# Optimization experiments

Hardware: AMD Instinct MI355X
Metric: run time of the kernel (lower is better)

## Reference

```python
import jax, jax.numpy as jnp
import numpy as np

BETA = 0.25
EPS = 1e-12  # matches torch F.normalize eps


def _normalize(x):
    # L2-normalize along last dim, matching F.normalize(x, dim=1)
    n = jnp.linalg.norm(x, axis=-1, keepdims=True)
    return x / jnp.maximum(n, EPS)


def setup_inputs() -> dict:
    key = jax.random.key(0)
    k1, k2 = jax.random.split(key)
    B, C, H, W = 32, 256, 32, 32
    num_embed = 8192
    z = jax.random.normal(k1, (B, C, H, W), dtype=jnp.float32)
    # codebook initialized uniform(-1/K, 1/K) as in the module
    embed_weight = jax.random.uniform(
        k2, (num_embed, C), minval=-1.0 / num_embed, maxval=1.0 / num_embed,
        dtype=jnp.float32)
    return {"z": z, "embed_weight": embed_weight}


def reference(z, embed_weight):
    B, C, H, W = z.shape
    sg = jax.lax.stop_gradient
    zt = jnp.transpose(z, (0, 2, 3, 1))           # [B, H, W, C]
    zf = zt.reshape(-1, C)                         # [N, C]
    # cosine distance (dot of normalized vectors); z side is detached
    zn = sg(_normalize(zf))                        # [N, C]
    cn = _normalize(embed_weight)                  # [K, C]
    dist = jnp.einsum('nd,kd->nk', zn, cn)         # [N, K]
    encoding_indices = jnp.argmax(dist, axis=1)    # [N]
    z_q = embed_weight[encoding_indices].reshape(zt.shape)  # [B, H, W, C]
    loss = (BETA * jnp.mean((sg(z_q) - zt) ** 2)
            + jnp.mean((z_q - sg(zt)) ** 2))
    z_q_st = zt + sg(z_q - zt)                     # straight-through
    out = jnp.transpose(z_q_st, (0, 3, 1, 2))      # [B, C, H, W]
    return out, loss, encoding_indices
```

## Files before the change

### kernel.cpp

```cpp
#include <hip/hip_runtime.h>

#define NROWS 32768
#define CDIM  256
#define KCODES 8192
#define HWPB  1024
#define OUT_ELEMS 8388608

typedef unsigned short ushort_t;
typedef unsigned int uint_t;
typedef __attribute__((ext_vector_type(8))) __bf16 bf16x8;
typedef __attribute__((ext_vector_type(4))) float f32x4;
typedef __attribute__((ext_vector_type(8))) ushort_t us8;
typedef __attribute__((ext_vector_type(4))) ushort_t us4;

#define RESCORE_THRESH 3.0e-4f

__device__ __forceinline__ ushort_t f2bf(float f) {
  uint_t u = __float_as_uint(f);
  return (ushort_t)((u + 0x7fffu + ((u >> 16) & 1u)) >> 16);
}
__device__ __forceinline__ float bf2f(ushort_t s) {
  return __uint_as_float(((uint_t)s) << 16);
}

__global__ __launch_bounds__(256) void vq_invnorm_kernel(
    const float* __restrict__ e, float* __restrict__ invn) {
  const int row  = blockIdx.x * 4 + (threadIdx.x >> 6);
  const int lane = threadIdx.x & 63;
  const float4 v = *reinterpret_cast<const float4*>(e + (size_t)row * CDIM + lane * 4);
  float s = v.x * v.x + v.y * v.y + v.z * v.z + v.w * v.w;
  #pragma unroll
  for (int o = 32; o > 0; o >>= 1) s += __shfl_down(s, o);
  if (lane == 0) invn[row] = 1.0f / fmaxf(sqrtf(s), 1e-12f);
}

__global__ __launch_bounds__(256) void vq_prep_b_kernel(
    const float* __restrict__ e, ushort_t* __restrict__ B2,
    float* __restrict__ invn) {
  const int k  = blockIdx.x * 4 + (threadIdx.x >> 6);
  const int ln = threadIdx.x & 63;
  const float4 v = reinterpret_cast<const float4*>(e + (size_t)k * CDIM)[ln];
  us4 hi, lo;
  const float vv[4] = {v.x, v.y, v.z, v.w};
  float s = 0.f;
  #pragma unroll
  for (int i = 0; i < 4; ++i) {
    ushort_t h = f2bf(vv[i]);
    hi[i] = h;
    lo[i] = f2bf(vv[i] - bf2f(h));
    s += vv[i] * vv[i];
  }
  *reinterpret_cast<us4*>(B2 + (size_t)k * 512 + ln * 4)       = hi;
  *reinterpret_cast<us4*>(B2 + (size_t)k * 512 + 256 + ln * 4) = lo;
  #pragma unroll
  for (int o = 32; o > 0; o >>= 1) s += __shfl_down(s, o);
  if (ln == 0) invn[k] = 1.0f / fmaxf(sqrtf(s), 1e-12f);
}

__global__ __launch_bounds__(256) void vq_prep_a_kernel(
    const float* __restrict__ z, ushort_t* __restrict__ A2) {
  __shared__ float zt[64][65];
  const int t    = threadIdx.x;
  const int bidx = blockIdx.x;
  const int b    = bidx >> 6;
  const int cblk = (bidx & 63) >> 4;
  const int hwb  = bidx & 15;
  const int c0   = cblk * 64;
  const int hw0  = hwb * 64;
  #pragma unroll
  for (int rep = 0; rep < 16; ++rep) {
    const int idx = rep * 256 + t;
    const int cc = idx >> 6, hh = idx & 63;
    zt[cc][hh] = z[(size_t)(b * 256 + c0 + cc) * 1024 + hw0 + hh];
  }
  __syncthreads();
  const int r = t >> 2, q = t & 3;
  const int n = b * 1024 + hw0 + r;
  us8 hi0, hi1, lo0, lo1;
  #pragma unroll
  for (int m2 = 0; m2 < 16; ++m2) {
    const float v = zt[q * 16 + m2][r];
    const ushort_t h = f2bf(v);
    const ushort_t l = f2bf(v - bf2f(h));
    if (m2 < 8) { hi0[m2] = h; lo0[m2] = l; } else { hi1[m2 - 8] = h; lo1[m2 - 8] = l; }
  }
  ushort_t* hrow = A2 + (size_t)n * 512 + c0 + q * 16;
  ushort_t* lrow = A2 + (size_t)n * 512 + 256 + c0 + q * 16;
  *reinterpret_cast<us8*>(hrow)     = hi0;
  *reinterpret_cast<us8*>(hrow + 8) = hi1;
  *reinterpret_cast<us8*>(lrow)     = lo0;
  *reinterpret_cast<us8*>(lrow + 8) = lo1;
}

__global__ __launch_bounds__(256, 2) void vq_mfma_kernel(
    const ushort_t* __restrict__ A2, const ushort_t* __restrict__ B2,
    const float* __restrict__ invn,
    float* __restrict__ partV1, int* __restrict__ partI1,
    float* __restrict__ partV2) {
  __shared__ __align__(16) char As[2][16384];
  __shared__ __align__(16) char Bs[2][16384];

  const int t = threadIdx.x;
  const int w = t >> 6, l = t & 63;
  const int wr = w >> 1, wc = w & 1;
  const int lane15 = l & 15, kg = l >> 4;
  const int m0 = blockIdx.x * 128;
  const int cg = blockIdx.y;

  const int lr = l >> 3;
  const int lc = (l & 7) ^ lr;

  const ushort_t* aRow = A2 + (size_t)(m0 + w * 8 + lr) * 512 + lc * 8;
  const ushort_t* bRow = B2 + (size_t)(cg * 1024 + w * 8 + lr) * 512 + lc * 8;
  const int ldsOff = (w * 8) * 128;

  auto stage = [&](int step, int buf) {
    const int nt = step / 12, kc = step % 12;
    const int seg = kc >> 2, rem = (kc & 3) * 64;
    const int aoff = (seg == 1 ? 256 : 0) + rem;
    const int boff = (seg == 2 ? 256 : 0) + rem;
    const size_t bNt = (size_t)nt * (128 * 512);
    #pragma unroll
    for (int p = 0; p < 4; ++p) {
      __builtin_amdgcn_global_load_lds(
          (const __attribute__((address_space(1))) void*)(aRow + (size_t)p * (32 * 512) + aoff),
          (__attribute__((address_space(3))) void*)(As[buf] + p * 32 * 128 + ldsOff), 16, 0, 0);
      __builtin_amdgcn_global_load_lds(
          (const __attribute__((address_space(1))) void*)(bRow + bNt + (size_t)p * (32 * 512) + boff),
          (__attribute__((address_space(3))) void*)(Bs[buf] + p * 32 * 128 + ldsOff), 16, 0, 0);
    }
  };

  float bv[16], b2v[16]; int bi[16];
  #pragma unroll
  for (int iq = 0; iq < 16; ++iq) { bv[iq] = -3.4e38f; b2v[iq] = -3.4e38f; bi[iq] = 0; }

  stage(0, 0);

  int step = 0;
  for (int nt = 0; nt < 8; ++nt) {
    const int nbase = cg * 1024 + nt * 128;
    f32x4 acc[4][4];
    #pragma unroll
    for (int i = 0; i < 4; ++i)
      #pragma unroll
      for (int j = 0; j < 4; ++j) acc[i][j] = (f32x4){0.f, 0.f, 0.f, 0.f};

    for (int kc = 0; kc < 12; ++kc, ++step) {
      const int buf = step & 1;
      __syncthreads();
      if (step + 1 < 96) stage(step + 1, buf ^ 1);

      const char* Ab = As[buf];
      const char* Bb = Bs[buf];
      #pragma unroll
      for (int kk = 0; kk < 2; ++kk) {
        bf16x8 af[4], bfr[4];
        const int sw = kk * 64 + kg * 16;
        const int sx = (lane15 & 7) << 4;
        #pragma unroll
        for (int i = 0; i < 4; ++i)
          af[i] = *reinterpret_cast<const bf16x8*>(
              Ab + (wr * 64 + i * 16 + lane15) * 128 + (sw ^ sx));
        #pragma unroll
        for (int j = 0; j < 4; ++j)
          bfr[j] = *reinterpret_cast<const bf16x8*>(
              Bb + (wc * 64 + j * 16 + lane15) * 128 + (sw ^ sx));
        #pragma unroll
        for (int i = 0; i < 4; ++i)
          #pragma unroll
          for (int j = 0; j < 4; ++j)
            acc[i][j] = __builtin_amdgcn_mfma_f32_16x16x32_bf16(af[i], bfr[j], acc[i][j], 0, 0, 0);
      }
    }

    float inv4[4];
    #pragma unroll
    for (int j = 0; j < 4; ++j) inv4[j] = invn[nbase + wc * 64 + j * 16 + lane15];
    #pragma unroll
    for (int i = 0; i < 4; ++i)
      #pragma unroll
      for (int q = 0; q < 4; ++q) {
        const int iq = i * 4 + q;
        #pragma unroll
        for (int j = 0; j < 4; ++j) {
          const float v = acc[i][j][q] * inv4[j];
          const int k = nbase + wc * 64 + j * 16 + lane15;
          if (v > bv[iq]) { b2v[iq] = bv[iq]; bv[iq] = v; bi[iq] = k; }
          else if (v > b2v[iq]) b2v[iq] = v;
        }
      }
  }

  #pragma unroll
  for (int m = 1; m < 16; m <<= 1) {
    #pragma unroll
    for (int iq = 0; iq < 16; ++iq) {
      const float ov = __shfl_xor(bv[iq], m);
      const int   oi = __shfl_xor(bi[iq], m);
      const float o2 = __shfl_xor(b2v[iq], m);
      const float n2 = fmaxf(fmaxf(b2v[iq], o2), fminf(bv[iq], ov));
      if (ov > bv[iq] || (ov == bv[iq] && oi < bi[iq])) { bv[iq] = ov; bi[iq] = oi; }
      b2v[iq] = n2;
    }
  }

  __syncthreads();
  float* lv1 = reinterpret_cast<float*>(As[0]);
  float* lv2 = lv1 + 128;
  int*   li1 = reinterpret_cast<int*>(lv2 + 128);
  if (wc == 1 && lane15 == 0) {
    #pragma unroll
    for (int i = 0; i < 4; ++i)
      #pragma unroll
      for (int q = 0; q < 4; ++q) {
        const int rl = wr * 64 + i * 16 + kg * 4 + q;
        lv1[rl] = bv[i * 4 + q]; lv2[rl] = b2v[i * 4 + q]; li1[rl] = bi[i * 4 + q];
      }
  }
  __syncthreads();
  if (wc == 0 && lane15 == 0) {
    #pragma unroll
    for (int i = 0; i < 4; ++i)
      #pragma unroll
      for (int q = 0; q < 4; ++q) {
        const int iq = i * 4 + q;
        const int rl = wr * 64 + i * 16 + kg * 4 + q;
        const float ov = lv1[rl]; const float o2 = lv2[rl]; const int oi = li1[rl];
        const float n2 = fmaxf(fmaxf(b2v[iq], o2), fminf(bv[iq], ov));
        float v1 = bv[iq]; int i1 = bi[iq];
        if (ov > v1 || (ov == v1 && oi < i1)) { v1 = ov; i1 = oi; }
        const size_t g = (size_t)cg * NROWS + m0 + rl;
        partV1[g] = v1; partI1[g] = i1; partV2[g] = n2;
      }
  }
}

__global__ __launch_bounds__(256) void vq_merge_flag_kernel(
    const float* __restrict__ partV1, const int* __restrict__ partI1,
    const float* __restrict__ partV2,
    int* __restrict__ final_idx, int* __restrict__ flag, int* __restrict__ cnt) {
  const int n = blockIdx.x * 256 + threadIdx.x;
  float v1 = partV1[n]; int i1 = partI1[n]; float v2 = partV2[n];
  #pragma unroll
  for (int cg = 1; cg < 8; ++cg) {
    const float pv1 = partV1[(size_t)cg * NROWS + n];
    const int   pi1 = partI1[(size_t)cg * NROWS + n];
    const float pv2 = partV2[(size_t)cg * NROWS + n];
    const float n2 = fmaxf(fmaxf(v2, pv2), fminf(v1, pv1));
    if (pv1 > v1) { v1 = pv1; i1 = pi1; }
    v2 = n2;
  }
  final_idx[n] = i1;
  if (v1 - v2 < RESCORE_THRESH) {
    const int p = atomicAdd(cnt, 1);
    flag[p] = n;
  }
}

__global__ __launch_bounds__(256) void vq_rescore_kernel(
    const float* __restrict__ z, const float* __restrict__ e,
    const float* __restrict__ invn, const int* __restrict__ cnt,
    const int* __restrict__ flag, int* __restrict__ final_idx) {
  __shared__ float zr[8][256];
  __shared__ int rows[8];
  __shared__ float redv[8][4];
  __shared__ int   redi[8][4];
  const int t = threadIdx.x;
  const int total = *cnt;
  for (int base = blockIdx.x * 8; base < total; base += gridDim.x * 8) {
    const int nr = min(8, total - base);
    __syncthreads();
    if (t < 8) rows[t] = (base + t < total) ? flag[base + t] : flag[base];
    __syncthreads();
    for (int rr = 0; rr < 8; ++rr) {
      if (rr < nr) {
        const int n = rows[rr];
        const int b = n >> 10, hw = n & 1023;
        zr[rr][t] = z[(size_t)b * 262144 + (size_t)t * 1024 + hw];
      } else {
        zr[rr][t] = 0.f;
      }
    }
    __syncthreads();
    float bvv[8]; int bii[8];
    #pragma unroll
    for (int rr = 0; rr < 8; ++rr) { bvv[rr] = -3.4e38f; bii[rr] = 0; }
    for (int jj = 0; jj < 32; ++jj) {
      const int k = t * 32 + jj;
      const float4* er = reinterpret_cast<const float4*>(e + (size_t)k * CDIM);
      float d[8];
      #pragma unroll
      for (int rr = 0; rr < 8; ++rr) d[rr] = 0.f;
      for (int c4 = 0; c4 < 64; ++c4) {
        const float4 ev = er[c4];
        #pragma unroll
        for (int rr = 0; rr < 8; ++rr) {
          d[rr] = fmaf(ev.x, zr[rr][c4 * 4 + 0], d[rr]);
          d[rr] = fmaf(ev.y, zr[rr][c4 * 4 + 1], d[rr]);
          d[rr] = fmaf(ev.z, zr[rr][c4 * 4 + 2], d[rr]);
          d[rr] = fmaf(ev.w, zr[rr][c4 * 4 + 3], d[rr]);
        }
      }
      const float inv = invn[k];
      #pragma unroll
      for (int rr = 0; rr < 8; ++rr) {
        const float v = d[rr] * inv;
        if (v > bvv[rr]) { bvv[rr] = v; bii[rr] = k; }
      }
    }
    #pragma unroll
    for (int m = 1; m < 64; m <<= 1) {
      #pragma unroll
      for (int rr = 0; rr < 8; ++rr) {
        const float ov = __shfl_xor(bvv[rr], m);
        const int   oi = __shfl_xor(bii[rr], m);
        if (ov > bvv[rr] || (ov == bvv[rr] && oi < bii[rr])) { bvv[rr] = ov; bii[rr] = oi; }
      }
    }
    if ((t & 63) == 0) {
      #pragma unroll
      for (int rr = 0; rr < 8; ++rr) { redv[rr][t >> 6] = bvv[rr]; redi[rr][t >> 6] = bii[rr]; }
    }
    __syncthreads();
    if (t < nr) {
      float v = redv[t][0]; int i = redi[t][0];
      #pragma unroll
      for (int ww = 1; ww < 4; ++ww) {
        if (redv[t][ww] > v || (redv[t][ww] == v && redi[t][ww] < i)) { v = redv[t][ww]; i = redi[t][ww]; }
      }
      final_idx[rows[t]] = i;
    }
  }
}

__global__ __launch_bounds__(256) void vq_gather_loss2_kernel(
    const float* __restrict__ z, const float* __restrict__ e,
    const int* __restrict__ final_idx,
    float* __restrict__ out, float* __restrict__ lossacc) {
  __shared__ int sidx[64];
  const int t  = threadIdx.x;
  const int n0 = blockIdx.x * 64;
  if (t < 64) {
    const int id = final_idx[n0 + t];
    sidx[t] = id;
    out[OUT_ELEMS + 1 + n0 + t] = (float)id;
  }
  __syncthreads();
  const int b    = n0 >> 10;
  const int hw0  = n0 & 1023;
  const int nsub = t & 63;
  const int cg   = t >> 6;
  const float* erow = e + (size_t)sidx[nsub] * CDIM;
  float lsum = 0.f;
  for (int c = cg; c < CDIM; c += 4) {
    const float  v   = erow[c];
    const size_t off = (size_t)b * (CDIM * HWPB) + (size_t)c * HWPB + hw0 + nsub;
    const float  d   = v - z[off];
    lsum += d * d;
    out[off] = v;
  }
  #pragma unroll
  for (int o = 32; o > 0; o >>= 1) lsum += __shfl_down(lsum, o);
  __shared__ float wsum[4];
  if ((t & 63) == 0) wsum[t >> 6] = lsum;
  __syncthreads();
  if (t == 0) atomicAdd(lossacc, wsum[0] + wsum[1] + wsum[2] + wsum[3]);
}

__global__ void vq_finalize_kernel(const float* __restrict__ lossacc,
                                   float* __restrict__ out) {
  out[OUT_ELEMS] = 1.25f * lossacc[0] / (float)OUT_ELEMS;
}

#define BM 128
#define BN 128
#define KC 16
#define KSPLIT 4

__global__ __launch_bounds__(256) void vq_dist_argmax_kernel(
    const float* __restrict__ z, const float* __restrict__ e,
    const float* __restrict__ invn,
    float* __restrict__ bestval, int* __restrict__ bestidx) {
  __shared__ float as[KC][BM];
  __shared__ float bs[KC][BN + 4];
  const int t  = threadIdx.x;
  const int tx = t & 15;
  const int ty = t >> 4;
  const int n0 = blockIdx.x * BM;
  const int b   = n0 >> 10;
  const int hw0 = n0 & 1023;
  const float* zbase = z + (size_t)b * (CDIM * HWPB) + hw0;
  const int kbeg = blockIdx.y * (KCODES / KSPLIT);
  float bv[8]; int bi[8];
  #pragma unroll
  for (int i = 0; i < 8; ++i) { bv[i] = -3.4e38f; bi[i] = 0; }
  const int a_lm4 = (t & 31) * 4;
  const int a_cc  = t >> 5;
  const int b_kk  = t >> 2;
  const int b_q4  = (t & 3) * 4;
  for (int kt = 0; kt < (KCODES / KSPLIT) / BN; ++kt) {
    const int k0 = kbeg + kt * BN;
    float acc[8][8];
    #pragma unroll
    for (int i = 0; i < 8; ++i)
      #pragma unroll
      for (int j = 0; j < 8; ++j) acc[i][j] = 0.f;
    for (int c0 = 0; c0 < CDIM; c0 += KC) {
      #pragma unroll
      for (int p = 0; p < 2; ++p) {
        const int cc = a_cc + 8 * p;
        const float4 v = *reinterpret_cast<const float4*>(
            zbase + (size_t)(c0 + cc) * HWPB + a_lm4);
        *reinterpret_cast<float4*>(&as[cc][a_lm4]) = v;
      }
      #pragma unroll
      for (int p = 0; p < 2; ++p) {
        const int kk = b_kk + 64 * p;
        const float4 v = *reinterpret_cast<const float4*>(
            e + (size_t)(k0 + kk) * CDIM + c0 + b_q4);
        bs[b_q4 + 0][kk] = v.x;
        bs[b_q4 + 1][kk] = v.y;
        bs[b_q4 + 2][kk] = v.z;
        bs[b_q4 + 3][kk] = v.w;
      }
      __syncthreads();
      #pragma unroll
      for (int cc = 0; cc < KC; ++cc) {
        const float4 a0 = *reinterpret_cast<const float4*>(&as[cc][ty * 8]);
        const float4 a1 = *reinterpret_cast<const float4*>(&as[cc][ty * 8 + 4]);
        const float4 b0 = *reinterpret_cast<const float4*>(&bs[cc][tx * 4]);
        const float4 b1 = *reinterpret_cast<const float4*>(&bs[cc][64 + tx * 4]);
        const float a[8]  = {a0.x, a0.y, a0.z, a0.w, a1.x, a1.y, a1.z, a1.w};
        const float bb[8] = {b0.x, b0.y, b0.z, b0.w, b1.x, b1.y, b1.z, b1.w};
        #pragma unroll
        for (int i = 0; i < 8; ++i)
          #pragma unroll
          for (int j = 0; j < 8; ++j)
            acc[i][j] = fmaf(a[i], bb[j], acc[i][j]);
      }
      __syncthreads();
    }
    #pragma unroll
    for (int j = 0; j < 8; ++j) {
      const int k = k0 + ((j < 4) ? (tx * 4 + j) : (64 + tx * 4 + (j - 4)));
      const float inv = invn[k];
      #pragma unroll
      for (int i = 0; i < 8; ++i) {
        const float v = acc[i][j] * inv;
        if (v > bv[i]) { bv[i] = v; bi[i] = k; }
      }
    }
  }
  #pragma unroll
  for (int m = 1; m < 16; m <<= 1) {
    #pragma unroll
    for (int i = 0; i < 8; ++i) {
      const float vo = __shfl_xor(bv[i], m);
      const int   io = __shfl_xor(bi[i], m);
      if (vo > bv[i] || (vo == bv[i] && io < bi[i])) { bv[i] = vo; bi[i] = io; }
    }
  }
  if (tx == 0) {
    #pragma unroll
    for (int i = 0; i < 8; ++i) {
      bestval[blockIdx.y * NROWS + n0 + ty * 8 + i] = bv[i];
      bestidx[blockIdx.y * NROWS + n0 + ty * 8 + i] = bi[i];
    }
  }
}

__global__ __launch_bounds__(256) void vq_gather_loss_kernel(
    const float* __restrict__ z, const float* __restrict__ e,
    const float* __restrict__ bestval, const int* __restrict__ bestidx,
    float* __restrict__ out, float* __restrict__ lossacc) {
  __shared__ int sidx[64];
  const int t  = threadIdx.x;
  const int n0 = blockIdx.x * 64;
  if (t < 64) {
    const int n = n0 + t;
    float best = bestval[n];
    int   bid  = bestidx[n];
    #pragma unroll
    for (int p = 1; p < KSPLIT; ++p) {
      const float v = bestval[p * NROWS + n];
      const int  id = bestidx[p * NROWS + n];
      if (v > best) { best = v; bid = id; }
    }
    sidx[t] = bid;
    out[OUT_ELEMS + 1 + n] = (float)bid;
  }
  __syncthreads();
  const int b    = n0 >> 10;
  const int hw0  = n0 & 1023;
  const int nsub = t & 63;
  const int cg   = t >> 6;
  const float* erow = e + (size_t)sidx[nsub] * CDIM;
  float lsum = 0.f;
  for (int c = cg; c < CDIM; c += 4) {
    const float  v   = erow[c];
    const size_t off = (size_t)b * (CDIM * HWPB) + (size_t)c * HWPB + hw0 + nsub;
    const float  d   = v - z[off];
    lsum += d * d;
    out[off] = v;
  }
  #pragma unroll
  for (int o = 32; o > 0; o >>= 1) lsum += __shfl_down(lsum, o);
  __shared__ float wsum[4];
  if ((t & 63) == 0) wsum[t >> 6] = lsum;
  __syncthreads();
  if (t == 0) atomicAdd(lossacc, wsum[0] + wsum[1] + wsum[2] + wsum[3]);
}

extern "C" void kernel_launch(void* const* d_in, const int* in_sizes, int n_in,
                              void* d_out, int out_size, void* d_ws, size_t ws_size,
                              hipStream_t stream) {
  const float* z = (const float*)d_in[0];
  const float* e = (const float*)d_in[1];
  float* out = (float*)d_out;

  const size_t szA2 = (size_t)NROWS * 512 * 2;
  const size_t szB2 = (size_t)KCODES * 512 * 2;
  const size_t szInv = KCODES * 4;
  const size_t szPart = (size_t)8 * NROWS * 4;
  const size_t need = szA2 + szB2 + szInv + 3 * szPart + 2 * (size_t)NROWS * 4 + 256;

  if (ws_size >= need) {
    char* p = (char*)d_ws;
    ushort_t* A2 = (ushort_t*)p;       p += szA2;
    ushort_t* B2 = (ushort_t*)p;       p += szB2;
    float* invn  = (float*)p;          p += szInv;
    float* partV1 = (float*)p;         p += szPart;
    float* partV2 = (float*)p;         p += szPart;
    int*   partI1 = (int*)p;           p += szPart;
    int*   final_idx = (int*)p;        p += (size_t)NROWS * 4;
    int*   flag = (int*)p;             p += (size_t)NROWS * 4;
    int*   cnt = (int*)p;
    float* lossacc = (float*)(cnt + 1);

    hipMemsetAsync(cnt, 0, 8, stream);
    vq_prep_b_kernel<<<KCODES / 4, 256, 0, stream>>>(e, B2, invn);
    vq_prep_a_kernel<<<2048, 256, 0, stream>>>(z, A2);
    dim3 grid(NROWS / 128, 8);
    vq_mfma_kernel<<<grid, 256, 0, stream>>>(A2, B2, invn, partV1, partI1, partV2);
    vq_merge_flag_kernel<<<NROWS / 256, 256, 0, stream>>>(partV1, partI1, partV2,
                                                          final_idx, flag, cnt);
    vq_rescore_kernel<<<256, 256, 0, stream>>>(z, e, invn, cnt, flag, final_idx);
    vq_gather_loss2_kernel<<<NROWS / 64, 256, 0, stream>>>(z, e, final_idx, out, lossacc);
    vq_finalize_kernel<<<1, 1, 0, stream>>>(lossacc, out);
  } else {
    float* invn    = (float*)d_ws;
    float* bestval = invn + KCODES;
    int*   bestidx = (int*)(bestval + KSPLIT * NROWS);
    float* lossacc = (float*)(bestidx + KSPLIT * NROWS);
    hipMemsetAsync(lossacc, 0, sizeof(float), stream);
    vq_invnorm_kernel<<<KCODES / 4, 256, 0, stream>>>(e, invn);
    dim3 grid(NROWS / BM, KSPLIT);
    vq_dist_argmax_kernel<<<grid, 256, 0, stream>>>(z, e, invn, bestval, bestidx);
    vq_gather_loss_kernel<<<NROWS / 64, 256, 0, stream>>>(z, e, bestval, bestidx,
                                                          out, lossacc);
    vq_finalize_kernel<<<1, 1, 0, stream>>>(lossacc, out);
  }
}
```

Before: 1.349 ms.

## Restructure MFMA argmax kernel with fragment-ordered A and 4-stage B pipeline

The z-side bf16 hi/lo split is now written in an MFMA-fragment-ordered layout, so each wave loads its A fragments straight from global memory instead of staging them through LDS. The distance kernel grows to 512 threads with 256x256 tiles, a 4-deep LDS ring for codebook tiles tracked by vmcnt waits rather than per-step barriers, raised MFMA priority, and a per-tile argmax reduction through LDS. The gather/loss kernel is rewritten to one row per thread with float4 codebook reads. The risks are heavy global-load traffic for A, 140KB of dynamic shared memory, which limits occupancy to one block per CU, and register pressure from the 8x4 accumulator array.

```diff
diff --git a/kernel.cpp b/kernel.cpp
--- a/kernel.cpp
+++ b/kernel.cpp
@@ -58,7 +58,7 @@
 }
 
 __global__ __launch_bounds__(256) void vq_prep_a_kernel(
-    const float* __restrict__ z, ushort_t* __restrict__ A2) {
+    const float* __restrict__ z, char* __restrict__ A2f) {
   __shared__ float zt[64][65];
   const int t    = threadIdx.x;
   const int bidx = blockIdx.x;
@@ -74,8 +74,12 @@
     zt[cc][hh] = z[(size_t)(b * 256 + c0 + cc) * 1024 + hw0 + hh];
   }
   __syncthreads();
-  const int r = t >> 2, q = t & 3;
-  const int n = b * 1024 + hw0 + r;
+  const int q = t >> 6, r = t & 63;
+  const int n   = b * 1024 + hw0 + r;
+  const int R16 = n >> 4, l15 = n & 15;
+  const int cb  = c0 + q * 16;
+  const int kc  = cb >> 5;
+  const int kg0 = (cb >> 3) & 3;
   us8 hi0, hi1, lo0, lo1;
   #pragma unroll
   for (int m2 = 0; m2 < 16; ++m2) {
@@ -84,155 +88,147 @@
     const ushort_t l = f2bf(v - bf2f(h));
     if (m2 < 8) { hi0[m2] = h; lo0[m2] = l; } else { hi1[m2 - 8] = h; lo1[m2 - 8] = l; }
   }
-  ushort_t* hrow = A2 + (size_t)n * 512 + c0 + q * 16;
-  ushort_t* lrow = A2 + (size_t)n * 512 + 256 + c0 + q * 16;
-  *reinterpret_cast<us8*>(hrow)     = hi0;
-  *reinterpret_cast<us8*>(hrow + 8) = hi1;
-  *reinterpret_cast<us8*>(lrow)     = lo0;
-  *reinterpret_cast<us8*>(lrow + 8) = lo1;
-}
-
-__global__ __launch_bounds__(256, 2) void vq_mfma_kernel(
-    const ushort_t* __restrict__ A2, const ushort_t* __restrict__ B2,
+  const size_t base = (size_t)(R16 * 16 + kc) * 1024 + (size_t)(((kg0) << 4) | l15) * 16;
+  *reinterpret_cast<us8*>(A2f + base)              = hi0;
+  *reinterpret_cast<us8*>(A2f + base + 256)        = hi1;
+  *reinterpret_cast<us8*>(A2f + base + 8192)       = lo0;
+  *reinterpret_cast<us8*>(A2f + base + 8192 + 256) = lo1;
+}
+
+__global__ __launch_bounds__(512) void vq_mfma_kernel(
+    const char* __restrict__ A2f, const ushort_t* __restrict__ B2,
     const float* __restrict__ invn,
     float* __restrict__ partV1, int* __restrict__ partI1,
     float* __restrict__ partV2) {
-  __shared__ __align__(16) char As[2][16384];
-  __shared__ __align__(16) char Bs[2][16384];
+  extern __shared__ char smem[];
 
   const int t = threadIdx.x;
   const int w = t >> 6, l = t & 63;
-  const int wr = w >> 1, wc = w & 1;
-  const int lane15 = l & 15, kg = l >> 4;
-  const int m0 = blockIdx.x * 128;
+  const int wr = w >> 2, wc = w & 3;
+  const int l15 = l & 15, kg = l >> 4;
+  const int m0 = blockIdx.x * 256;
   const int cg = blockIdx.y;
 
-  const int lr = l >> 3;
-  const int lc = (l & 7) ^ lr;
-
-  const ushort_t* aRow = A2 + (size_t)(m0 + w * 8 + lr) * 512 + lc * 8;
-  const ushort_t* bRow = B2 + (size_t)(cg * 1024 + w * 8 + lr) * 512 + lc * 8;
-  const int ldsOff = (w * 8) * 128;
-
-  auto stage = [&](int step, int buf) {
-    const int nt = step / 12, kc = step % 12;
-    const int seg = kc >> 2, rem = (kc & 3) * 64;
-    const int aoff = (seg == 1 ? 256 : 0) + rem;
-    const int boff = (seg == 2 ? 256 : 0) + rem;
-    const size_t bNt = (size_t)nt * (128 * 512);
-    #pragma unroll
-    for (int p = 0; p < 4; ++p) {
+  const int rowB  = l >> 2;
+  const int slotB = (l & 3) ^ ((l >> 2) & 3);
+  const int rdoffB = l15 * 64 + ((kg ^ (l15 & 3)) << 4);
+  const char* aFbase = A2f + (size_t)m0 * 1024 + (size_t)wr * 131072 + (size_t)l * 16;
+
+  float* candV1 = reinterpret_cast<float*>(smem + 131072);
+  int*   candI1 = reinterpret_cast<int*>(smem + 135168);
+  float* candV2 = reinterpret_cast<float*>(smem + 139264);
+
+  auto stageB = [&](int s3) {
+    if (s3 >= 96) return;
+    const int nt3 = s3 / 24;
+    const int kc3 = s3 - nt3 * 24;
+    const int boff = (kc3 < 8) ? kc3 * 32
+                   : (kc3 < 16 ? (kc3 - 8) * 32 : 256 + (kc3 - 16) * 32);
+    const int bufb = (s3 & 3) * 32768 + w * 4096;
+    const ushort_t* src = B2 +
+        (size_t)((cg << 10) + nt3 * 256 + wc * 64 + rowB) * 512 + slotB * 8 + boff;
+    #pragma unroll
+    for (int u = 0; u < 4; ++u) {
       __builtin_amdgcn_global_load_lds(
-          (const __attribute__((address_space(1))) void*)(aRow + (size_t)p * (32 * 512) + aoff),
-          (__attribute__((address_space(3))) void*)(As[buf] + p * 32 * 128 + ldsOff), 16, 0, 0);
-      __builtin_amdgcn_global_load_lds(
-          (const __attribute__((address_space(1))) void*)(bRow + bNt + (size_t)p * (32 * 512) + boff),
-          (__attribute__((address_space(3))) void*)(Bs[buf] + p * 32 * 128 + ldsOff), 16, 0, 0);
+          (const __attribute__((address_space(1))) void*)(src + (size_t)u * (16 * 512)),
+          (__attribute__((address_space(3))) void*)(smem + bufb + u * 1024 + l * 16),
+          16, 0, 0);
     }
   };
 
-  float bv[16], b2v[16]; int bi[16];
-  #pragma unroll
-  for (int iq = 0; iq < 16; ++iq) { bv[iq] = -3.4e38f; b2v[iq] = -3.4e38f; bi[iq] = 0; }
-
-  stage(0, 0);
-
-  int step = 0;
-  for (int nt = 0; nt < 8; ++nt) {
-    const int nbase = cg * 1024 + nt * 128;
-    f32x4 acc[4][4];
-    #pragma unroll
-    for (int i = 0; i < 4; ++i)
+  stageB(0); stageB(1); stageB(2);
+
+  float rv1 = -3.4e38f, rv2 = -3.4e38f; int ri1 = 0;
+
+  for (int nt = 0; nt < 4; ++nt) {
+    const int nbase = (cg << 10) + nt * 256;
+    f32x4 acc[8][4];
+    #pragma unroll
+    for (int i = 0; i < 8; ++i)
       #pragma unroll
       for (int j = 0; j < 4; ++j) acc[i][j] = (f32x4){0.f, 0.f, 0.f, 0.f};
 
-    for (int kc = 0; kc < 12; ++kc, ++step) {
-      const int buf = step & 1;
-      __syncthreads();
-      if (step + 1 < 96) stage(step + 1, buf ^ 1);
-
-      const char* Ab = As[buf];
-      const char* Bb = Bs[buf];
-      #pragma unroll
-      for (int kk = 0; kk < 2; ++kk) {
-        bf16x8 af[4], bfr[4];
-        const int sw = kk * 64 + kg * 16;
-        const int sx = (lane15 & 7) << 4;
-        #pragma unroll
-        for (int i = 0; i < 4; ++i)
-          af[i] = *reinterpret_cast<const bf16x8*>(
-              Ab + (wr * 64 + i * 16 + lane15) * 128 + (sw ^ sx));
+    for (int kc = 0; kc < 24; ++kc) {
+      const int s = nt * 24 + kc;
+      stageB(s + 3);
+      asm volatile("s_waitcnt vmcnt(8)" ::: "memory");
+
+      const int kcA = (kc < 16) ? kc : kc - 16;
+      const char* aa = aFbase + (size_t)kcA * 1024;
+      bf16x8 af[8];
+      #pragma unroll
+      for (int i = 0; i < 8; ++i)
+        af[i] = *reinterpret_cast<const bf16x8*>(aa + (size_t)i * 16384);
+
+      const char* bb = smem + (s & 3) * 32768 + w * 4096 + rdoffB;
+      bf16x8 bfr[4];
+      #pragma unroll
+      for (int j = 0; j < 4; ++j)
+        bfr[j] = *reinterpret_cast<const bf16x8*>(bb + j * 1024);
+
+      __builtin_amdgcn_s_setprio(1);
+      #pragma unroll
+      for (int i = 0; i < 8; ++i)
         #pragma unroll
         for (int j = 0; j < 4; ++j)
-          bfr[j] = *reinterpret_cast<const bf16x8*>(
-              Bb + (wc * 64 + j * 16 + lane15) * 128 + (sw ^ sx));
+          acc[i][j] = __builtin_amdgcn_mfma_f32_16x16x32_bf16(af[i], bfr[j], acc[i][j], 0, 0, 0);
+      __builtin_amdgcn_s_setprio(0);
+    }
+
+    float inv[4];
+    #pragma unroll
+    for (int j = 0; j < 4; ++j) inv[j] = invn[nbase + wc * 64 + j * 16 + l15];
+
+    #pragma unroll
+    for (int i = 0; i < 8; ++i) {
+      #pragma unroll
+      for (int q = 0; q < 4; ++q) {
+        float v1 = acc[i][0][q] * inv[0];
+        int   i1 = nbase + wc * 64 + l15;
+        float v2 = -3.4e38f;
         #pragma unroll
-        for (int i = 0; i < 4; ++i)
-          #pragma unroll
-          for (int j = 0; j < 4; ++j)
-            acc[i][j] = __builtin_amdgcn_mfma_f32_16x16x32_bf16(af[i], bfr[j], acc[i][j], 0, 0, 0);
-      }
-    }
-
-    float inv4[4];
-    #pragma unroll
-    for (int j = 0; j < 4; ++j) inv4[j] = invn[nbase + wc * 64 + j * 16 + lane15];
-    #pragma unroll
-    for (int i = 0; i < 4; ++i)
-      #pragma unroll
-      for (int q = 0; q < 4; ++q) {
-        const int iq = i * 4 + q;
+        for (int j = 1; j < 4; ++j) {
+          const float v = acc[i][j][q] * inv[j];
+          const int   c = nbase + wc * 64 + j * 16 + l15;
+          if (v > v1) { v2 = v1; v1 = v; i1 = c; }
+          else if (v > v2) v2 = v;
+        }
         #pragma unroll
-        for (int j = 0; j < 4; ++j) {
-          const float v = acc[i][j][q] * inv4[j];
-          const int k = nbase + wc * 64 + j * 16 + lane15;
-          if (v > bv[iq]) { b2v[iq] = bv[iq]; bv[iq] = v; bi[iq] = k; }
-          else if (v > b2v[iq]) b2v[iq] = v;
+        for (int m = 1; m < 16; m <<= 1) {
+          const float ov = __shfl_xor(v1, m);
+          const int   oi = __shfl_xor(i1, m);
+          const float o2 = __shfl_xor(v2, m);
+          const float n2 = fmaxf(fmaxf(v2, o2), fminf(v1, ov));
+          if (ov > v1 || (ov == v1 && oi < i1)) { v1 = ov; i1 = oi; }
+          v2 = n2;
         }
-      }
-  }
-
-  #pragma unroll
-  for (int m = 1; m < 16; m <<= 1) {
-    #pragma unroll
-    for (int iq = 0; iq < 16; ++iq) {
-      const float ov = __shfl_xor(bv[iq], m);
-      const int   oi = __shfl_xor(bi[iq], m);
-      const float o2 = __shfl_xor(b2v[iq], m);
-      const float n2 = fmaxf(fmaxf(b2v[iq], o2), fminf(bv[iq], ov));
-      if (ov > bv[iq] || (ov == bv[iq] && oi < bi[iq])) { bv[iq] = ov; bi[iq] = oi; }
-      b2v[iq] = n2;
-    }
-  }
-
-  __syncthreads();
-  float* lv1 = reinterpret_cast<float*>(As[0]);
-  float* lv2 = lv1 + 128;
-  int*   li1 = reinterpret_cast<int*>(lv2 + 128);
-  if (wc == 1 && lane15 == 0) {
-    #pragma unroll
-    for (int i = 0; i < 4; ++i)
-      #pragma unroll
-      for (int q = 0; q < 4; ++q) {
-        const int rl = wr * 64 + i * 16 + kg * 4 + q;
-        lv1[rl] = bv[i * 4 + q]; lv2[rl] = b2v[i * 4 + q]; li1[rl] = bi[i * 4 + q];
-      }
-  }
-  __syncthreads();
-  if (wc == 0 && lane15 == 0) {
-    #pragma unroll
-    for (int i = 0; i < 4; ++i)
-      #pragma unroll
-      for (int q = 0; q < 4; ++q) {
-        const int iq = i * 4 + q;
-        const int rl = wr * 64 + i * 16 + kg * 4 + q;
-        const float ov = lv1[rl]; const float o2 = lv2[rl]; const int oi = li1[rl];
-        const float n2 = fmaxf(fmaxf(b2v[iq], o2), fminf(bv[iq], ov));
-        float v1 = bv[iq]; int i1 = bi[iq];
-        if (ov > v1 || (ov == v1 && oi < i1)) { v1 = ov; i1 = oi; }
-        const size_t g = (size_t)cg * NROWS + m0 + rl;
-        partV1[g] = v1; partI1[g] = i1; partV2[g] = n2;
-      }
+        if (l15 == 0) {
+          const int row = wr * 128 + i * 16 + kg * 4 + q;
+          candV1[wc * 256 + row] = v1;
+          candI1[wc * 256 + row] = i1;
+          candV2[wc * 256 + row] = v2;
+        }
+      }
+    }
+    asm volatile("s_waitcnt lgkmcnt(0)" ::: "memory");
+    __builtin_amdgcn_s_barrier();
+    if (t < 256) {
+      #pragma unroll
+      for (int wcc = 0; wcc < 4; ++wcc) {
+        const float v1c = candV1[wcc * 256 + t];
+        const int   i1c = candI1[wcc * 256 + t];
+        const float v2c = candV2[wcc * 256 + t];
+        const float n2 = fmaxf(fmaxf(rv2, v2c), fminf(rv1, v1c));
+        if (v1c > rv1 || (v1c == rv1 && i1c < ri1)) { rv1 = v1c; ri1 = i1c; }
+        rv2 = n2;
+      }
+    }
+    __builtin_amdgcn_s_barrier();
+  }
+
+  if (t < 256) {
+    const size_t g = (size_t)cg * NROWS + m0 + t;
+    partV1[g] = rv1; partI1[g] = ri1; partV2[g] = rv2;
   }
 }
 
@@ -334,31 +330,28 @@
   }
 }
 
-__global__ __launch_bounds__(256) void vq_gather_loss2_kernel(
+__global__ __launch_bounds__(256) void vq_gather_loss3_kernel(
     const float* __restrict__ z, const float* __restrict__ e,
     const int* __restrict__ final_idx,
     float* __restrict__ out, float* __restrict__ lossacc) {
-  __shared__ int sidx[64];
-  const int t  = threadIdx.x;
-  const int n0 = blockIdx.x * 64;
-  if (t < 64) {
-    const int id = final_idx[n0 + t];
-    sidx[t] = id;
-    out[OUT_ELEMS + 1 + n0 + t] = (float)id;
-  }
-  __syncthreads();
-  const int b    = n0 >> 10;
-  const int hw0  = n0 & 1023;
-  const int nsub = t & 63;
-  const int cg   = t >> 6;
-  const float* erow = e + (size_t)sidx[nsub] * CDIM;
+  const int t = threadIdx.x;
+  const int n = blockIdx.x * 256 + t;
+  const int b = n >> 10, hw = n & 1023;
+  const int id = final_idx[n];
+  out[OUT_ELEMS + 1 + n] = (float)id;
+  const float4* er = reinterpret_cast<const float4*>(e + (size_t)id * CDIM);
+  const size_t zb = (size_t)b * 262144 + hw;
   float lsum = 0.f;
-  for (int c = cg; c < CDIM; c += 4) {
-    const float  v   = erow[c];
-    const size_t off = (size_t)b * (CDIM * HWPB) + (size_t)c * HWPB + hw0 + nsub;
-    const float  d   = v - z[off];
-    lsum += d * d;
-    out[off] = v;
+  for (int c4 = 0; c4 < 64; ++c4) {
+    const float4 ev = er[c4];
+    const float evv[4] = {ev.x, ev.y, ev.z, ev.w};
+    #pragma unroll
+    for (int u = 0; u < 4; ++u) {
+      const size_t off = zb + (size_t)(c4 * 4 + u) * 1024;
+      const float d = evv[u] - z[off];
+      lsum += d * d;
+      out[off] = evv[u];
+    }
   }
   #pragma unroll
   for (int o = 32; o > 0; o >>= 1) lsum += __shfl_down(lsum, o);
@@ -519,7 +512,7 @@
   const float* e = (const float*)d_in[1];
   float* out = (float*)d_out;
 
-  const size_t szA2 = (size_t)NROWS * 512 * 2;
+  const size_t szA2 = (size_t)2048 * 16 * 1024;
   const size_t szB2 = (size_t)KCODES * 512 * 2;
   const size_t szInv = KCODES * 4;
   const size_t szPart = (size_t)8 * NROWS * 4;
@@ -527,7 +520,7 @@
 
   if (ws_size >= need) {
     char* p = (char*)d_ws;
-    ushort_t* A2 = (ushort_t*)p;       p += szA2;
+    char* A2f = p;                     p += szA2;
     ushort_t* B2 = (ushort_t*)p;       p += szB2;
     float* invn  = (float*)p;          p += szInv;
     float* partV1 = (float*)p;         p += szPart;
@@ -540,13 +533,13 @@
 
     hipMemsetAsync(cnt, 0, 8, stream);
     vq_prep_b_kernel<<<KCODES / 4, 256, 0, stream>>>(e, B2, invn);
-    vq_prep_a_kernel<<<2048, 256, 0, stream>>>(z, A2);
-    dim3 grid(NROWS / 128, 8);
-    vq_mfma_kernel<<<grid, 256, 0, stream>>>(A2, B2, invn, partV1, partI1, partV2);
+    vq_prep_a_kernel<<<2048, 256, 0, stream>>>(z, A2f);
+    dim3 grid(NROWS / 256, 8);
+    vq_mfma_kernel<<<grid, 512, 143360, stream>>>(A2f, B2, invn, partV1, partI1, partV2);
     vq_merge_flag_kernel<<<NROWS / 256, 256, 0, stream>>>(partV1, partI1, partV2,
                                                           final_idx, flag, cnt);
     vq_rescore_kernel<<<256, 256, 0, stream>>>(z, e, invn, cnt, flag, final_idx);
-    vq_gather_loss2_kernel<<<NROWS / 64, 256, 0, stream>>>(z, e, final_idx, out, lossacc);
+    vq_gather_loss3_kernel<<<NROWS / 256, 256, 0, stream>>>(z, e, final_idx, out, lossacc);
     vq_finalize_kernel<<<1, 1, 0, stream>>>(lossacc, out);
   } else {
     float* invn    = (float*)d_ws;
```

Result: slower. 1.531 ms (+13.5%).

## Prefetch two stages ahead with explicit vmcnt waits and raw barriers

Applied to the files above, without the earlier changes.

The double-buffered pipeline now issues the first two stages up front. Each iteration waits with s_waitcnt vmcnt(8), so only the older stage's async global-to-LDS loads must land, then uses a raw s_barrier instead of __syncthreads. After the MFMA loop a second barrier releases the buffer, which is then refilled with stage s+2. This keeps one stage of loads in flight during compute to hide global latency. It relies on exact vmcnt counting: each stage issues 8 loads, and any other outstanding loads would break that count. The final barrier also drops the implicit waitcnt.

```diff
diff --git a/kernel.cpp b/kernel.cpp
--- a/kernel.cpp
+++ b/kernel.cpp
@@ -103,7 +103,7 @@
   const int t = threadIdx.x;
   const int w = t >> 6, l = t & 63;
   const int wr = w >> 1, wc = w & 1;
-  const int lane15 = l & 15, kg = l >> 4;
+  const int l15 = l & 15, kg = l >> 4;
   const int m0 = blockIdx.x * 128;
   const int cg = blockIdx.y;
 
@@ -114,12 +114,12 @@
   const ushort_t* bRow = B2 + (size_t)(cg * 1024 + w * 8 + lr) * 512 + lc * 8;
   const int ldsOff = (w * 8) * 128;
 
-  auto stage = [&](int step, int buf) {
-    const int nt = step / 12, kc = step % 12;
-    const int seg = kc >> 2, rem = (kc & 3) * 64;
+  auto stage = [&](int s3, int buf) {
+    const int nt3 = s3 / 12, kc3 = s3 - nt3 * 12;
+    const int seg = kc3 >> 2, rem = (kc3 & 3) * 64;
     const int aoff = (seg == 1 ? 256 : 0) + rem;
     const int boff = (seg == 2 ? 256 : 0) + rem;
-    const size_t bNt = (size_t)nt * (128 * 512);
+    const size_t bNt = (size_t)nt3 * (128 * 512);
     #pragma unroll
     for (int p = 0; p < 4; ++p) {
       __builtin_amdgcn_global_load_lds(
@@ -136,20 +136,26 @@
   for (int iq = 0; iq < 16; ++iq) { bv[iq] = -3.4e38f; b2v[iq] = -3.4e38f; bi[iq] = 0; }
 
   stage(0, 0);
-
-  int step = 0;
+  stage(1, 1);
+
+  int s = 0;
   for (int nt = 0; nt < 8; ++nt) {
-    const int nbase = cg * 1024 + nt * 128;
+    const int nbase = (cg << 10) + nt * 128;
     f32x4 acc[4][4];
     #pragma unroll
     for (int i = 0; i < 4; ++i)
       #pragma unroll
       for (int j = 0; j < 4; ++j) acc[i][j] = (f32x4){0.f, 0.f, 0.f, 0.f};
 
-    for (int kc = 0; kc < 12; ++kc, ++step) {
-      const int buf = step & 1;
-      __syncthreads();
-      if (step + 1 < 96) stage(step + 1, buf ^ 1);
+    for (int kc = 0; kc < 12; ++kc, ++s) {
+      const int buf = s & 1;
+      if (s < 95) {
+        asm volatile("s_waitcnt vmcnt(8)" ::: "memory");
+      } else {
+        asm volatile("s_waitcnt vmcnt(0)" ::: "memory");
+      }
+      __builtin_amdgcn_s_barrier();
+      __builtin_amdgcn_sched_barrier(0);
 
       const char* Ab = As[buf];
       const char* Bb = Bs[buf];
@@ -157,26 +163,30 @@
       for (int kk = 0; kk < 2; ++kk) {
         bf16x8 af[4], bfr[4];
         const int sw = kk * 64 + kg * 16;
-        const int sx = (lane15 & 7) << 4;
+        const int sx = (l15 & 7) << 4;
         #pragma unroll
         for (int i = 0; i < 4; ++i)
           af[i] = *reinterpret_cast<const bf16x8*>(
-              Ab + (wr * 64 + i * 16 + lane15) * 128 + (sw ^ sx));
+              Ab + (wr * 64 + i * 16 + l15) * 128 + (sw ^ sx));
         #pragma unroll
         for (int j = 0; j < 4; ++j)
           bfr[j] = *reinterpret_cast<const bf16x8*>(
-              Bb + (wc * 64 + j * 16 + lane15) * 128 + (sw ^ sx));
+              Bb + (wc * 64 + j * 16 + l15) * 128 + (sw ^ sx));
         #pragma unroll
         for (int i = 0; i < 4; ++i)
           #pragma unroll
           for (int j = 0; j < 4; ++j)
             acc[i][j] = __builtin_amdgcn_mfma_f32_16x16x32_bf16(af[i], bfr[j], acc[i][j], 0, 0, 0);
       }
+
+      __builtin_amdgcn_s_barrier();
+      __builtin_amdgcn_sched_barrier(0);
+      if (s + 2 < 96) stage(s + 2, buf);
     }
 
     float inv4[4];
     #pragma unroll
-    for (int j = 0; j < 4; ++j) inv4[j] = invn[nbase + wc * 64 + j * 16 + lane15];
+    for (int j = 0; j < 4; ++j) inv4[j] = invn[nbase + wc * 64 + j * 16 + l15];
     #pragma unroll
     for (int i = 0; i < 4; ++i)
       #pragma unroll
@@ -185,7 +195,7 @@
         #pragma unroll
         for (int j = 0; j < 4; ++j) {
           const float v = acc[i][j][q] * inv4[j];
-          const int k = nbase + wc * 64 + j * 16 + lane15;
+          const int k = nbase + wc * 64 + j * 16 + l15;
           if (v > bv[iq]) { b2v[iq] = bv[iq]; bv[iq] = v; bi[iq] = k; }
           else if (v > b2v[iq]) b2v[iq] = v;
         }
@@ -205,11 +215,11 @@
     }
   }
 
-  __syncthreads();
+  __builtin_amdgcn_s_barrier();
   float* lv1 = reinterpret_cast<float*>(As[0]);
   float* lv2 = lv1 + 128;
   int*   li1 = reinterpret_cast<int*>(lv2 + 128);
-  if (wc == 1 && lane15 == 0) {
+  if (wc == 1 && l15 == 0) {
     #pragma unroll
     for (int i = 0; i < 4; ++i)
       #pragma unroll
@@ -219,7 +229,7 @@
       }
   }
   __syncthreads();
-  if (wc == 0 && lane15 == 0) {
+  if (wc == 0 && l15 == 0) {
     #pragma unroll
     for (int i = 0; i < 4; ++i)
       #pragma unroll
```

Result: no change. 1.347 ms (-0.1%).
